# Optimization experiments

Measured on AMD Instinct MI355X. Metric: run time of the kernel, lower is better.

Reference implementation:

```python
import jax, jax.numpy as jnp
import numpy as np

NUM_HEADS = 8
D_HEAD = 64
LN_EPS = 1e-6


def _pad_idx(lengths, max_len):
    # flat indices into a [B*max_len, ...] dense buffer for each packed token
    return np.concatenate([b * max_len + np.arange(int(l)) for b, l in enumerate(lengths)])


def _layer_norm(x, scale, bias):
    mu = jnp.mean(x, axis=-1, keepdims=True)
    var = jnp.mean(jnp.square(x - mu), axis=-1, keepdims=True)
    return (x - mu) * jax.lax.rsqrt(var + LN_EPS) * scale + bias


def setup_inputs() -> dict:
    key = jax.random.key(0)
    ks = jax.random.split(key, 12)
    d_model, d_ff, H, dh = 512, 2048, NUM_HEADS, D_HEAD
    lengths = np.array([128 * (i + 1) for i in range(8)], dtype=np.int64)  # sum = 4608
    total = int(lengths.sum())
    s = 0.02
    return {
        "x": jax.random.normal(ks[0], (total, d_model), jnp.float32),
        "mem": jax.random.normal(ks[1], (total, d_model), jnp.float32),
        "lengths_x": lengths,
        "lengths_mem": lengths.copy(),
        "Wq": jax.random.normal(ks[2], (d_model, H * dh), jnp.float32) * s,
        "Wk": jax.random.normal(ks[3], (d_model, H * dh), jnp.float32) * s,
        "Wv": jax.random.normal(ks[4], (d_model, H * dh), jnp.float32) * s,
        "Wo": jax.random.normal(ks[5], (H * dh, d_model), jnp.float32) * s,
        "ln1_scale": jnp.ones((d_model,), jnp.float32),
        "ln1_bias": jnp.zeros((d_model,), jnp.float32),
        "W1": jax.random.normal(ks[6], (d_model, d_ff), jnp.float32) * s,
        "b1": jnp.zeros((d_ff,), jnp.float32),
        "W2": jax.random.normal(ks[7], (d_ff, d_model), jnp.float32) * s,
        "b2": jnp.zeros((d_model,), jnp.float32),
        "ln2_scale": jnp.ones((d_model,), jnp.float32),
        "ln2_bias": jnp.zeros((d_model,), jnp.float32),
    }


def reference(x, mem, lengths_x, lengths_mem, Wq, Wk, Wv, Wo,
              ln1_scale, ln1_bias, W1, b1, W2, b2, ln2_scale, ln2_bias):
    lx = np.asarray(lengths_x)
    lm = np.asarray(lengths_mem)
    B = lx.shape[0]
    Lx = int(lx.max())
    Lm = int(lm.max())
    H, dh = NUM_HEADS, D_HEAD

    idx_x = _pad_idx(lx, Lx)
    idx_m = _pad_idx(lm, Lm)

    def pad(packed, idx, B, L):
        dense = jnp.zeros((B * L,) + packed.shape[1:], packed.dtype).at[idx].set(packed)
        return dense.reshape((B, L) + packed.shape[1:])

    q = pad((x @ Wq).reshape(-1, H, dh), idx_x, B, Lx)   # [B, Lx, H, dh]
    k = pad((mem @ Wk).reshape(-1, H, dh), idx_m, B, Lm)  # [B, Lm, H, dh]
    v = pad((mem @ Wv).reshape(-1, H, dh), idx_m, B, Lm)

    e = jnp.einsum('bxhd,byhd->bhxy', q, k) / np.sqrt(dh)  # [B, H, Lx, Lm]
    # validity mask: (query pos < len_x) & (key pos < len_mem)
    mask = (np.arange(Lx)[None, :, None] < lx[:, None, None]) & \
           (np.arange(Lm)[None, None, :] < lm[:, None, None])
    mask = jnp.asarray(mask)[:, None, :, :]  # [B, 1, Lx, Lm]
    e = jnp.where(mask, e, jnp.float32(-1e30))  # finite -inf surrogate; identical softmax on valid rows
    alpha = jax.nn.softmax(e, axis=-1)
    out = jnp.einsum('bhxy,byhd->bxhd', alpha, v).reshape(B, Lx, H * dh)
    out = out @ Wo                                  # [B, Lx, d_model]
    out = out.reshape(B * Lx, -1)[idx_x]            # pack back to [total_x, d_model]

    h = _layer_norm(x + out, ln1_scale, ln1_bias)
    ffn = jax.nn.relu(h @ W1 + b1) @ W2 + b2
    return _layer_norm(h + ffn, ln2_scale, ln2_bias)
```

## Files before the change

kernel.cpp:

```cpp
#include <hip/hip_runtime.h>
#include <stdint.h>

typedef short bf8v __attribute__((ext_vector_type(8)));
typedef float f4v  __attribute__((ext_vector_type(4)));
typedef short s8v  __attribute__((ext_vector_type(8)));
typedef short s4v  __attribute__((ext_vector_type(4)));
typedef int   i2v  __attribute__((ext_vector_type(2)));

__device__ __forceinline__ float bf2f(short b){
  unsigned u = ((unsigned)(unsigned short)b) << 16;
  union { unsigned u; float f; } c; c.u = u; return c.f;
}
__device__ __forceinline__ short f2bf(float f){
  union { float f; unsigned u; } c; c.f = f;
  unsigned r = (c.u + 0x7FFFu + ((c.u >> 16) & 1u)) >> 16;
  return (short)r;
}
__device__ __forceinline__ void gload16(const short* g, short* l){
  __builtin_amdgcn_global_load_lds(
      (const __attribute__((address_space(1))) void*)g,
      (__attribute__((address_space(3))) void*)l, 16, 0, 0);
}

__global__ __launch_bounds__(256) void setup_kernel(
    const int* lx, const int* lm, int* meta,
    const float* __restrict__ Wq, const float* __restrict__ Wk,
    const float* __restrict__ Wv, const float* __restrict__ Wo,
    const float* __restrict__ W1, const float* __restrict__ W2,
    short* __restrict__ WqT, short* __restrict__ WkT,
    short* __restrict__ WvT, short* __restrict__ WoT,
    short* __restrict__ W1T, short* __restrict__ W2T){
  __shared__ int sjp[9], skvc[8];
  __shared__ float tile[32][33];
  int tid = threadIdx.x;
  int bid = blockIdx.x;

  if (bid == 0){
    if (tid == 0){
      int is64 = ((lx[1] | lx[3] | lx[5] | lx[7]) == 0) ? 1 : 0;
      int ox = 0, om = 0;
      for (int b = 0; b < 8; ++b){
        int a = is64 ? lx[2*b] : lx[b];
        int c = is64 ? lm[2*b] : lm[b];
        meta[b] = a; meta[8+b] = c;
        meta[16+b] = ox; meta[25+b] = om;
        ox += a; om += c;
      }
      meta[24] = ox; meta[33] = om;
      int jp = 0;
      for (int b = 0; b < 8; ++b){
        int Lm_ = meta[8+b];
        int kvc = (Lm_ + 255) / 256; if (kvc > 4) kvc = 4; if (kvc < 1) kvc = 1;
        int clen = (((Lm_ + kvc - 1) / kvc) + 31) & ~31;
        meta[34+b] = kvc; meta[42+b] = clen;
        meta[50+b] = jp;
        sjp[b] = jp; skvc[b] = kvc;
        int qt = (meta[b] + 63) / 64;
        jp += qt * kvc * 8;
      }
      meta[58] = jp;
      sjp[8] = jp;
    }
    __syncthreads();
    int njobs = sjp[8];
    for (int j = tid; j < njobs; j += blockDim.x){
      int b = 0;
      #pragma unroll
      for (int i = 1; i < 8; ++i) if (j >= sjp[i]) b = i;
      int local = j - sjp[b];
      int kvc = skvc[b];
      int h = local & 7;
      int r = local >> 3;
      int c = r % kvc;
      int qt = r / kvc;
      meta[64+j] = b | (h << 4) | (c << 7) | (qt << 11);
    }
    return;
  }

  int wbid = bid - 1;
  const float* W; short* WT; int K, N, t0;
  if      (wbid <  256){ W=Wq; WT=WqT; K=512;  N=512;  t0=0;    }
  else if (wbid <  512){ W=Wk; WT=WkT; K=512;  N=512;  t0=256;  }
  else if (wbid <  768){ W=Wv; WT=WvT; K=512;  N=512;  t0=512;  }
  else if (wbid < 1024){ W=Wo; WT=WoT; K=512;  N=512;  t0=768;  }
  else if (wbid < 2048){ W=W1; WT=W1T; K=512;  N=2048; t0=1024; }
  else                 { W=W2; WT=W2T; K=2048; N=512;  t0=2048; }
  int lt = wbid - t0;
  int ntn = N / 32;
  int tk = lt / ntn, tn = lt % ntn;
  int r0 = tid >> 5, c = tid & 31;
  #pragma unroll
  for (int i = 0; i < 4; ++i){
    int r = r0 + i*8;
    tile[r][c] = W[(long)(tk*32 + r)*N + tn*32 + c];
  }
  __syncthreads();
  #pragma unroll
  for (int i = 0; i < 4; ++i){
    int r = r0 + i*8;
    WT[(long)(tn*32 + r)*K + tk*32 + c] = f2bf(tile[c][r]);
  }
}

template<bool AF32>
__device__ __forceinline__ void stage_g64(const void* A, const short* Bt,
    long brow, long bcol, int M, int N, int K, int t,
    short* Als, short* Bls){
  int tid = threadIdx.x;
  {
    int row = tid >> 2, slot = tid & 3;
    int cg = slot ^ ((row >> 1) & 3);
    long ar = brow + row; if (ar >= M) ar = M - 1;
    if constexpr (AF32){
      const float* src = (const float*)A + ar*(long)K + t + cg*8;
      float4 f0 = *(const float4*)src;
      float4 f1 = *(const float4*)(src + 4);
      s8v o;
      o[0]=f2bf(f0.x); o[1]=f2bf(f0.y); o[2]=f2bf(f0.z); o[3]=f2bf(f0.w);
      o[4]=f2bf(f1.x); o[5]=f2bf(f1.y); o[6]=f2bf(f1.z); o[7]=f2bf(f1.w);
      *(s8v*)&Als[tid*8] = o;
    } else {
      gload16((const short*)A + ar*(long)K + t + cg*8, &Als[tid*8]);
    }
  }
  #pragma unroll
  for (int i = 0; i < 2; ++i){
    int cc = i*256 + tid;
    int row = cc >> 2, slot = cc & 3;
    int cg = slot ^ ((row >> 1) & 3);
    long br = bcol + row; if (br >= N) br = N - 1;
    gload16(Bt + br*(long)K + t + cg*8, &Bls[cc*8]);
  }
}

template<bool AF32>
__device__ __forceinline__ void gemm_core64(const void* A, const short* Bt,
    short* __restrict__ Cb, const float* __restrict__ bias,
    int M, int N, int K, int k0, int klen,
    float scale, int relu, int colmajor,
    long brow, long bcol, short* Als, short* Bls){
  int tid = threadIdx.x;
  int lane = tid & 63, w = tid >> 6;
  int wcol = w * 32;
  int l15 = lane & 15, l4 = lane >> 4;

  f4v acc[4][2];
  #pragma unroll
  for (int m = 0; m < 4; ++m)
    #pragma unroll
    for (int n = 0; n < 2; ++n) acc[m][n] = (f4v){0.f,0.f,0.f,0.f};

  int nt = klen / 32;
  stage_g64<AF32>(A, Bt, brow, bcol, M, N, K, k0, Als, Bls);
  for (int t = 0; t < nt; ++t){
    __syncthreads();
    if (t + 1 < nt)
      stage_g64<AF32>(A, Bt, brow, bcol, M, N, K, k0 + (t+1)*32,
                      Als + ((t+1)&1)*2048, Bls + ((t+1)&1)*4096);
    const short* Ab = Als + (t&1)*2048;
    const short* Bb = Bls + (t&1)*4096;
    bf8v a[4], b[2];
    #pragma unroll
    for (int m = 0; m < 4; ++m){
      int row = m*16 + l15;
      a[m] = *(const bf8v*)&Ab[row*32 + (l4 ^ ((row >> 1) & 3))*8];
    }
    #pragma unroll
    for (int n = 0; n < 2; ++n){
      int row = wcol + n*16 + l15;
      b[n] = *(const bf8v*)&Bb[row*32 + (l4 ^ ((row >> 1) & 3))*8];
    }
    #pragma unroll
    for (int m = 0; m < 4; ++m){
      acc[m][0] = __builtin_amdgcn_mfma_f32_16x16x32_bf16(a[m], b[0], acc[m][0], 0, 0, 0);
      acc[m][1] = __builtin_amdgcn_mfma_f32_16x16x32_bf16(a[m], b[1], acc[m][1], 0, 0, 0);
    }
  }

  #pragma unroll
  for (int m = 0; m < 4; ++m){
    #pragma unroll
    for (int n = 0; n < 2; ++n){
      long col = bcol + wcol + n*16 + l15;
      float bi = (bias != nullptr && col < N) ? bias[col] : 0.f;
      #pragma unroll
      for (int j = 0; j < 4; ++j){
        long row = brow + m*16 + 4*l4 + j;
        if (row < M && col < N){
          float v = acc[m][n][j] * scale + bi;
          if (relu) v = fmaxf(v, 0.f);
          Cb[colmajor ? (col*(long)M + row) : (row*(long)N + col)] = f2bf(v);
        }
      }
    }
  }
}

__global__ __launch_bounds__(256) void gemm64(
    const short* __restrict__ A, const short* __restrict__ Bt,
    short* __restrict__ C, const float* __restrict__ bias,
    int M, int N, int K, int klen, float scale, int relu, int colmajor){
  __shared__ __align__(16) short Als[2*64*32];
  __shared__ __align__(16) short Bls[2*128*32];
  int chunk = blockIdx.z;
  gemm_core64<false>(A, Bt, C + (long)chunk * M * N, bias, M, N, K, chunk*klen, klen,
                     scale, relu, colmajor,
                     (long)blockIdx.y * 64, (long)blockIdx.x * 128, Als, Bls);
}

__global__ __launch_bounds__(256) void gemm_qkv(
    const float* __restrict__ x, const float* __restrict__ mem,
    const short* __restrict__ WqT, const short* __restrict__ WkT,
    const short* __restrict__ WvT,
    short* __restrict__ Qb, short* __restrict__ Kbf, short* __restrict__ Vtb,
    int total){
  __shared__ __align__(16) short Als[2*64*32];
  __shared__ __align__(16) short Bls[2*128*32];
  int seg = blockIdx.x >> 2;
  const float* A  = (seg == 0) ? x : mem;
  const short* Bt = (seg == 0) ? WqT : ((seg == 1) ? WkT : WvT);
  short* C        = (seg == 0) ? Qb  : ((seg == 1) ? Kbf : Vtb);
  float scale     = (seg == 0) ? 0.125f : 1.f;
  int colmajor    = (seg == 2);
  gemm_core64<true>(A, Bt, C, nullptr, total, 512, 512, 0, 512, scale, 0, colmajor,
                    (long)blockIdx.y * 64, (long)(blockIdx.x & 3) * 128, Als, Bls);
}

__global__ __launch_bounds__(256) void attn_kernel(
    const short* __restrict__ Q, const short* __restrict__ Kb,
    const short* __restrict__ Vt, short* __restrict__ Ob,
    short* __restrict__ Opart, float* __restrict__ mlpart,
    const int* __restrict__ meta, int total){
  __shared__ __align__(16) short Kls[2][32*64];
  __shared__ __align__(16) short Vls[2][64*32];
  __shared__ __align__(16) short Pls[4][16*32];
  int tid = threadIdx.x;
  int lane = tid & 63, w = tid >> 6;
  int l15 = lane & 15, l4 = lane >> 4;
  int njobs = meta[58];

  for (int j = blockIdx.x; j < njobs; j += gridDim.x){
    int word = meta[64+j];
    int b = word & 15, h = (word >> 4) & 7, c = (word >> 7) & 15, qt = word >> 11;
    int Lx = meta[b], Lm = meta[8+b];
    int ox = meta[16+b], om = meta[25+b];
    int kvc = meta[34+b], clen = meta[42+b];
    int c0 = c * clen;
    int cend = c0 + clen; if (cend > Lm) cend = Lm;
    int nt = (cend - c0 + 31) / 32;
    int qbase = qt*64 + w*16;

    __syncthreads();

    #define ATTN_STAGE(T, BUF)                                                  \
      {                                                                         \
        int kv0_ = c0 + (T)*32;                                                 \
        int kr = tid >> 3, ks_ = tid & 7;                                       \
        int cgk = ks_ ^ (kr & 7);                                               \
        int ktok = kv0_ + kr; if (ktok >= Lm) ktok = Lm - 1;                    \
        gload16(Kb + (long)(om + ktok)*512 + h*64 + cgk*8, &Kls[BUF][tid*8]);   \
        int vr = tid >> 2, vs = tid & 3;                                        \
        int cgv = vs ^ (vr & 3);                                                \
        int vkv = kv0_ + cgv*8; if (vkv + 8 > Lm) vkv = Lm - 8;                 \
        gload16(Vt + (long)(h*64 + vr)*total + om + vkv, &Vls[BUF][tid*8]);     \
      }

    ATTN_STAGE(0, 0)

    int qr = qbase + l15;
    const short* qp = Q + (long)(ox + (qr < Lx ? qr : Lx - 1))*512 + h*64 + l4*8;
    bf8v aq0 = *(const bf8v*)qp;
    bf8v aq1 = *(const bf8v*)(qp + 32);

    float mrun = -1e30f, lrun = 0.f;
    f4v o[4];
    #pragma unroll
    for (int n = 0; n < 4; ++n) o[n] = (f4v){0.f,0.f,0.f,0.f};

    for (int t = 0; t < nt; ++t){
      __syncthreads();
      if (t + 1 < nt) ATTN_STAGE(t+1, (t+1)&1)
      int buf = t & 1;
      int kv0 = c0 + t*32;

      f4v s[2];
      #pragma unroll
      for (int n = 0; n < 2; ++n){
        int krow = n*16 + l15;
        bf8v k0 = *(const bf8v*)&Kls[buf][krow*64 + ((l4    ) ^ (krow & 7))*8];
        bf8v k1 = *(const bf8v*)&Kls[buf][krow*64 + ((4 + l4) ^ (krow & 7))*8];
        f4v z = (f4v){0.f,0.f,0.f,0.f};
        z = __builtin_amdgcn_mfma_f32_16x16x32_bf16(k0, aq0, z, 0, 0, 0);
        z = __builtin_amdgcn_mfma_f32_16x16x32_bf16(k1, aq1, z, 0, 0, 0);
        s[n] = z;
      }
      if (kv0 + 32 > cend){
        #pragma unroll
        for (int n = 0; n < 2; ++n){
          int kvb = kv0 + n*16 + 4*l4;
          #pragma unroll
          for (int jj = 0; jj < 4; ++jj)
            if (kvb + jj >= cend) s[n][jj] = -1e30f;
        }
      }
      float m1 = fmaxf(fmaxf(fmaxf(s[0][0], s[0][1]), fmaxf(s[0][2], s[0][3])),
                       fmaxf(fmaxf(s[1][0], s[1][1]), fmaxf(s[1][2], s[1][3])));
      m1 = fmaxf(m1, __shfl_xor(m1, 16, 64));
      m1 = fmaxf(m1, __shfl_xor(m1, 32, 64));
      float mnew = fmaxf(mrun, m1);
      float sc = __expf(mrun - mnew);
      mrun = mnew;
      float rs = 0.f;
      #pragma unroll
      for (int n = 0; n < 2; ++n)
        #pragma unroll
        for (int jj = 0; jj < 4; ++jj){
          float p = __expf(s[n][jj] - mnew);
          s[n][jj] = p; rs += p;
        }
      rs += __shfl_xor(rs, 16, 64);
      rs += __shfl_xor(rs, 32, 64);
      lrun = lrun * sc + rs;
      #pragma unroll
      for (int n = 0; n < 4; ++n) o[n] *= sc;

      #pragma unroll
      for (int n = 0; n < 2; ++n){
        unsigned r0, r1;
        asm("v_cvt_pk_bf16_f32 %0, %1, %2" : "=v"(r0) : "v"(s[n][0]), "v"(s[n][1]));
        asm("v_cvt_pk_bf16_f32 %0, %1, %2" : "=v"(r1) : "v"(s[n][2]), "v"(s[n][3]));
        i2v pr; pr[0] = (int)r0; pr[1] = (int)r1;
        int cs = (n*4 + l4) ^ ((l15 & 3) << 1);
        *(i2v*)&Pls[w][l15*32 + cs*4] = pr;
      }
      bf8v pb = *(const bf8v*)&Pls[w][l15*32 + (((2*l4) ^ ((l15 & 3) << 1))*4)];

      #pragma unroll
      for (int n2 = 0; n2 < 4; ++n2){
        int vrow = n2*16 + l15;
        bf8v vv = *(const bf8v*)&Vls[buf][vrow*32 + ((l4 ^ (vrow & 3))*8)];
        o[n2] = __builtin_amdgcn_mfma_f32_16x16x32_bf16(vv, pb, o[n2], 0, 0, 0);
      }
    }
    #undef ATTN_STAGE

    if (qr < Lx){
      if (kvc == 1){
        float inv = 1.f / lrun;
        long obase = (long)(ox + qr)*512 + h*64;
        #pragma unroll
        for (int n2 = 0; n2 < 4; ++n2){
          s4v ov;
          #pragma unroll
          for (int jj = 0; jj < 4; ++jj) ov[jj] = f2bf(o[n2][jj] * inv);
          *(s4v*)&Ob[obase + n2*16 + l4*4] = ov;
        }
      } else {
        long slot = ((long)(ox + qr)*8 + h)*4 + c;
        #pragma unroll
        for (int n2 = 0; n2 < 4; ++n2){
          s4v ov;
          #pragma unroll
          for (int jj = 0; jj < 4; ++jj) ov[jj] = f2bf(o[n2][jj]);
          *(s4v*)&Opart[slot*64 + n2*16 + l4*4] = ov;
        }
        if (l4 == 0){
          float2 ml; ml.x = mrun; ml.y = lrun;
          *(float2*)&mlpart[slot*2] = ml;
        }
      }
    }
  }
}

__global__ __launch_bounds__(256) void attn_combine(
    const short* __restrict__ Opart, const float* __restrict__ mlpart,
    short* __restrict__ Ob, const int* __restrict__ meta, int total){
  int w = threadIdx.x >> 6, lane = threadIdx.x & 63;
  int row = blockIdx.x*4 + w;
  if (row >= total) return;
  int b = 0;
  #pragma unroll
  for (int i = 1; i < 8; ++i) if (row >= meta[16+i]) b = i;
  int kvc = meta[34+b];
  if (kvc <= 1) return;
  for (int h = 0; h < 8; ++h){
    long sbase = ((long)row*8 + h)*4;
    float m_ = -1e30f;
    for (int c = 0; c < kvc; ++c) m_ = fmaxf(m_, mlpart[(sbase+c)*2]);
    float num = 0.f, den = 0.f;
    for (int c = 0; c < kvc; ++c){
      float mc = mlpart[(sbase+c)*2];
      float lc = mlpart[(sbase+c)*2 + 1];
      float wgt = __expf(mc - m_);
      num += wgt * bf2f(Opart[(sbase+c)*64 + lane]);
      den += wgt * lc;
    }
    Ob[(long)row*512 + h*64 + lane] = f2bf(num / den);
  }
}

__global__ __launch_bounds__(256) void ln_fuse(
    const float* __restrict__ Af, const short* __restrict__ Ab,
    const short* __restrict__ PartB, int nparts, long pstride,
    const float* __restrict__ bias,
    const float* __restrict__ gamma, const float* __restrict__ beta,
    short* __restrict__ outb, float* __restrict__ outf, int rows){
  int w = threadIdx.x >> 6, lane = threadIdx.x & 63;
  long row = (long)blockIdx.x * 4 + w;
  if (row >= rows) return;
  int c0 = lane * 8;
  long base = row * 512 + c0;
  float v[8];
  if (Af){
    float4 f0 = *(const float4*)(Af + base);
    float4 f1 = *(const float4*)(Af + base + 4);
    v[0]=f0.x; v[1]=f0.y; v[2]=f0.z; v[3]=f0.w;
    v[4]=f1.x; v[5]=f1.y; v[6]=f1.z; v[7]=f1.w;
  } else {
    s8v a = *(const s8v*)(Ab + base);
    #pragma unroll
    for (int j = 0; j < 8; ++j) v[j] = bf2f(a[j]);
  }
  for (int c = 0; c < nparts; ++c){
    s8v pv = *(const s8v*)(PartB + c*pstride + base);
    #pragma unroll
    for (int j = 0; j < 8; ++j) v[j] += bf2f(pv[j]);
  }
  if (bias){
    #pragma unroll
    for (int j = 0; j < 8; ++j) v[j] += bias[c0 + j];
  }
  float sum = 0.f;
  #pragma unroll
  for (int j = 0; j < 8; ++j) sum += v[j];
  #pragma unroll
  for (int m = 1; m < 64; m <<= 1) sum += __shfl_xor(sum, m, 64);
  float mu = sum * (1.f/512.f);
  float q = 0.f;
  #pragma unroll
  for (int j = 0; j < 8; ++j){ float d = v[j] - mu; q += d*d; }
  #pragma unroll
  for (int m = 1; m < 64; m <<= 1) q += __shfl_xor(q, m, 64);
  float rs = rsqrtf(q * (1.f/512.f) + 1e-6f);
  float ov[8];
  #pragma unroll
  for (int j = 0; j < 8; ++j)
    ov[j] = (v[j] - mu) * rs * gamma[c0 + j] + beta[c0 + j];
  if (outb){
    s8v os;
    #pragma unroll
    for (int j = 0; j < 8; ++j) os[j] = f2bf(ov[j]);
    *(s8v*)(outb + base) = os;
  }
  if (outf){
    float4 f0 = {ov[0], ov[1], ov[2], ov[3]};
    float4 f1 = {ov[4], ov[5], ov[6], ov[7]};
    *(float4*)(outf + base) = f0;
    *(float4*)(outf + base + 4) = f1;
  }
}

extern "C" void kernel_launch(void* const* d_in, const int* in_sizes, int n_in,
                              void* d_out, int out_size, void* d_ws, size_t ws_size,
                              hipStream_t stream){
  (void)n_in; (void)out_size; (void)ws_size;
  const float* x   = (const float*)d_in[0];
  const float* mem = (const float*)d_in[1];
  const int*   lxr = (const int*)d_in[2];
  const int*   lmr = (const int*)d_in[3];
  const float* Wq  = (const float*)d_in[4];
  const float* Wk  = (const float*)d_in[5];
  const float* Wv  = (const float*)d_in[6];
  const float* Wo  = (const float*)d_in[7];
  const float* g1  = (const float*)d_in[8];
  const float* be1 = (const float*)d_in[9];
  const float* W1  = (const float*)d_in[10];
  const float* b1  = (const float*)d_in[11];
  const float* W2  = (const float*)d_in[12];
  const float* b2  = (const float*)d_in[13];
  const float* g2  = (const float*)d_in[14];
  const float* be2 = (const float*)d_in[15];
  float* out = (float*)d_out;

  int total = in_sizes[0] / 512;
  if (total <= 0) return;
  long long n = (long long)total * 512;

  char* p = (char*)d_ws;
  int*   meta  = (int*)p;    p += 16384;
  short* Qb    = (short*)p;  p += n*2;
  short* Kbf   = (short*)p;  p += n*2;
  short* Vtb   = (short*)p;  p += n*2;
  short* attnb = (short*)p;  p += n*2;
  short* hb    = (short*)p;  p += n*2;
  short* ffn1  = (short*)p;  p += (long long)total*2048*2;
  short* Opart = (short*)p;  p += (long long)total*8*4*64*2;
  float* mlprt = (float*)p;  p += (long long)total*8*4*2*4;
  short* p_wo  = (short*)p;  p += n*4*2;
  short* p_ff  = (short*)p;  p += n*4*2;
  short* WqT   = (short*)p;  p += 512*512*2;
  short* WkT   = (short*)p;  p += 512*512*2;
  short* WvT   = (short*)p;  p += 512*512*2;
  short* WoT   = (short*)p;  p += 512*512*2;
  short* W1T   = (short*)p;  p += 2048*512*2;
  short* W2T   = (short*)p;  p += 512*2048*2;

  setup_kernel<<<dim3(1 + 3072), 256, 0, stream>>>(
      lxr, lmr, meta, Wq, Wk, Wv, Wo, W1, W2, WqT, WkT, WvT, WoT, W1T, W2T);

  int mt64 = (total + 63)/64;
  gemm_qkv<<<dim3(12, mt64), 256, 0, stream>>>(x, mem, WqT, WkT, WvT,
                                               Qb, Kbf, Vtb, total);

  attn_kernel<<<dim3(2048), 256, 0, stream>>>(Qb, Kbf, Vtb, attnb,
                                              Opart, mlprt, meta, total);
  attn_combine<<<dim3((unsigned)((total + 3)/4)), 256, 0, stream>>>(
      Opart, mlprt, attnb, meta, total);

  gemm64<<<dim3(4, mt64, 4), 256, 0, stream>>>(attnb, WoT, p_wo, nullptr,
                                               total, 512, 512, 128, 1.f, 0, 0);
  ln_fuse<<<dim3((unsigned)((total + 3)/4)), 256, 0, stream>>>(
      x, nullptr, p_wo, 4, n, nullptr, g1, be1, hb, nullptr, total);

  gemm64<<<dim3(16, mt64, 1), 256, 0, stream>>>(hb, W1T, ffn1, b1,
                                                total, 2048, 512, 512, 1.f, 1, 0);
  gemm64<<<dim3(4, mt64, 4), 256, 0, stream>>>(ffn1, W2T, p_ff, nullptr,
                                               total, 512, 2048, 512, 1.f, 0, 0);
  ln_fuse<<<dim3((unsigned)((total + 3)/4)), 256, 0, stream>>>(
      nullptr, hb, p_ff, 4, n, b2, g2, be2, nullptr, out, total);
}
```

Measured before the change: 178.1 us.

## Merge all stages into one cooperative persistent kernel with grid syncs

Replaces the chain of separate launches (weight transpose, QKV GEMM, attention, combine, Wo GEMM, LN, FFN GEMMs, LN) with a single cooperative persistent kernel. Blocks loop over the work items of each phase and use grid-wide syncs between phases. The goal is to remove per-launch overhead and the gaps between kernels. The Wo split-K factor also drops from 4 to 2. In exchange, the grid is capped at 1024 blocks, and grid syncs plus lower occupancy during heavy phases such as attention may cost throughput.

```diff
diff --git a/kernel.cpp b/kernel.cpp
--- a/kernel.cpp
+++ b/kernel.cpp
@@ -1,5 +1,8 @@
 #include <hip/hip_runtime.h>
+#include <hip/hip_cooperative_groups.h>
 #include <stdint.h>
+
+namespace cg = cooperative_groups;
 
 typedef short bf8v __attribute__((ext_vector_type(8)));
 typedef float f4v  __attribute__((ext_vector_type(4)));
@@ -22,26 +25,193 @@
       (__attribute__((address_space(3))) void*)l, 16, 0, 0);
 }
 
-__global__ __launch_bounds__(256) void setup_kernel(
-    const int* lx, const int* lm, int* meta,
-    const float* __restrict__ Wq, const float* __restrict__ Wk,
-    const float* __restrict__ Wv, const float* __restrict__ Wo,
-    const float* __restrict__ W1, const float* __restrict__ W2,
-    short* __restrict__ WqT, short* __restrict__ WkT,
-    short* __restrict__ WvT, short* __restrict__ WoT,
-    short* __restrict__ W1T, short* __restrict__ W2T){
-  __shared__ int sjp[9], skvc[8];
-  __shared__ float tile[32][33];
+struct MegaArgs {
+  const float* x; const float* mem;
+  const int* lx; const int* lm;
+  const float* Wq; const float* Wk; const float* Wv; const float* Wo;
+  const float* W1; const float* W2;
+  const float* g1; const float* be1; const float* b1;
+  const float* b2; const float* g2; const float* be2;
+  float* out;
+  int total;
+  int* meta;
+  short* Qb; short* Kbf; short* Vtb; short* attnb; short* hb; short* ffn1;
+  short* Opart; float* mlprt; short* p_wo; short* p_ff;
+  short* WqT; short* WkT; short* WvT; short* WoT; short* W1T; short* W2T;
+};
+
+template<bool AF32>
+__device__ __forceinline__ void stage_g64(const void* A, const short* Bt,
+    long brow, long bcol, int M, int N, int K, int t,
+    short* Als, short* Bls){
   int tid = threadIdx.x;
-  int bid = blockIdx.x;
+  {
+    int row = tid >> 2, slot = tid & 3;
+    int cg2 = slot ^ ((row >> 1) & 3);
+    long ar = brow + row; if (ar >= M) ar = M - 1;
+    if constexpr (AF32){
+      const float* src = (const float*)A + ar*(long)K + t + cg2*8;
+      float4 f0 = *(const float4*)src;
+      float4 f1 = *(const float4*)(src + 4);
+      s8v o;
+      o[0]=f2bf(f0.x); o[1]=f2bf(f0.y); o[2]=f2bf(f0.z); o[3]=f2bf(f0.w);
+      o[4]=f2bf(f1.x); o[5]=f2bf(f1.y); o[6]=f2bf(f1.z); o[7]=f2bf(f1.w);
+      *(s8v*)&Als[tid*8] = o;
+    } else {
+      gload16((const short*)A + ar*(long)K + t + cg2*8, &Als[tid*8]);
+    }
+  }
+  #pragma unroll
+  for (int i = 0; i < 2; ++i){
+    int cc = i*256 + tid;
+    int row = cc >> 2, slot = cc & 3;
+    int cg2 = slot ^ ((row >> 1) & 3);
+    long br = bcol + row; if (br >= N) br = N - 1;
+    gload16(Bt + br*(long)K + t + cg2*8, &Bls[cc*8]);
+  }
+}
+
+template<bool AF32>
+__device__ __forceinline__ void gemm_core64(const void* A, const short* Bt,
+    short* __restrict__ Cb, const float* __restrict__ bias,
+    int M, int N, int K, int k0, int klen,
+    float scale, int relu, int colmajor,
+    long brow, long bcol, short* Als, short* Bls){
+  int tid = threadIdx.x;
+  int lane = tid & 63, w = tid >> 6;
+  int wcol = w * 32;
+  int l15 = lane & 15, l4 = lane >> 4;
+
+  f4v acc[4][2];
+  #pragma unroll
+  for (int m = 0; m < 4; ++m)
+    #pragma unroll
+    for (int n = 0; n < 2; ++n) acc[m][n] = (f4v){0.f,0.f,0.f,0.f};
+
+  int nt = klen / 32;
+  stage_g64<AF32>(A, Bt, brow, bcol, M, N, K, k0, Als, Bls);
+  for (int t = 0; t < nt; ++t){
+    __syncthreads();
+    if (t + 1 < nt)
+      stage_g64<AF32>(A, Bt, brow, bcol, M, N, K, k0 + (t+1)*32,
+                      Als + ((t+1)&1)*2048, Bls + ((t+1)&1)*4096);
+    const short* Ab = Als + (t&1)*2048;
+    const short* Bb = Bls + (t&1)*4096;
+    bf8v a[4], b[2];
+    #pragma unroll
+    for (int m = 0; m < 4; ++m){
+      int row = m*16 + l15;
+      a[m] = *(const bf8v*)&Ab[row*32 + (l4 ^ ((row >> 1) & 3))*8];
+    }
+    #pragma unroll
+    for (int n = 0; n < 2; ++n){
+      int row = wcol + n*16 + l15;
+      b[n] = *(const bf8v*)&Bb[row*32 + (l4 ^ ((row >> 1) & 3))*8];
+    }
+    #pragma unroll
+    for (int m = 0; m < 4; ++m){
+      acc[m][0] = __builtin_amdgcn_mfma_f32_16x16x32_bf16(a[m], b[0], acc[m][0], 0, 0, 0);
+      acc[m][1] = __builtin_amdgcn_mfma_f32_16x16x32_bf16(a[m], b[1], acc[m][1], 0, 0, 0);
+    }
+  }
+
+  #pragma unroll
+  for (int m = 0; m < 4; ++m){
+    #pragma unroll
+    for (int n = 0; n < 2; ++n){
+      long col = bcol + wcol + n*16 + l15;
+      float bi = (bias != nullptr && col < N) ? bias[col] : 0.f;
+      #pragma unroll
+      for (int j = 0; j < 4; ++j){
+        long row = brow + m*16 + 4*l4 + j;
+        if (row < M && col < N){
+          float v = acc[m][n][j] * scale + bi;
+          if (relu) v = fmaxf(v, 0.f);
+          Cb[colmajor ? (col*(long)M + row) : (row*(long)N + col)] = f2bf(v);
+        }
+      }
+    }
+  }
+}
+
+__device__ __forceinline__ void ln_row(
+    const float* Af, const short* Ab, const short* PartB, int nparts,
+    long pstride, const float* bias, const float* gamma, const float* beta,
+    short* outb, float* outf, long row, int lane){
+  int c0 = lane * 8;
+  long base = row * 512 + c0;
+  float v[8];
+  if (Af){
+    float4 f0 = *(const float4*)(Af + base);
+    float4 f1 = *(const float4*)(Af + base + 4);
+    v[0]=f0.x; v[1]=f0.y; v[2]=f0.z; v[3]=f0.w;
+    v[4]=f1.x; v[5]=f1.y; v[6]=f1.z; v[7]=f1.w;
+  } else {
+    s8v a = *(const s8v*)(Ab + base);
+    #pragma unroll
+    for (int j = 0; j < 8; ++j) v[j] = bf2f(a[j]);
+  }
+  for (int c = 0; c < nparts; ++c){
+    s8v pv = *(const s8v*)(PartB + c*pstride + base);
+    #pragma unroll
+    for (int j = 0; j < 8; ++j) v[j] += bf2f(pv[j]);
+  }
+  if (bias){
+    #pragma unroll
+    for (int j = 0; j < 8; ++j) v[j] += bias[c0 + j];
+  }
+  float sum = 0.f;
+  #pragma unroll
+  for (int j = 0; j < 8; ++j) sum += v[j];
+  #pragma unroll
+  for (int m = 1; m < 64; m <<= 1) sum += __shfl_xor(sum, m, 64);
+  float mu = sum * (1.f/512.f);
+  float q = 0.f;
+  #pragma unroll
+  for (int j = 0; j < 8; ++j){ float d = v[j] - mu; q += d*d; }
+  #pragma unroll
+  for (int m = 1; m < 64; m <<= 1) q += __shfl_xor(q, m, 64);
+  float rs = rsqrtf(q * (1.f/512.f) + 1e-6f);
+  float ov[8];
+  #pragma unroll
+  for (int j = 0; j < 8; ++j)
+    ov[j] = (v[j] - mu) * rs * gamma[c0 + j] + beta[c0 + j];
+  if (outb){
+    s8v os;
+    #pragma unroll
+    for (int j = 0; j < 8; ++j) os[j] = f2bf(ov[j]);
+    *(s8v*)(outb + base) = os;
+  }
+  if (outf){
+    float4 f0 = {ov[0], ov[1], ov[2], ov[3]};
+    float4 f1 = {ov[4], ov[5], ov[6], ov[7]};
+    *(float4*)(outf + base) = f0;
+    *(float4*)(outf + base + 4) = f1;
+  }
+}
+
+__global__ __launch_bounds__(256, 4) void mega_kernel(MegaArgs A){
+  __shared__ __align__(16) char sm[24576];
+  short* Als = (short*)sm;
+  short* Bls = (short*)(sm + 8192);
+  cg::grid_group gg = cg::this_grid();
+
+  int tid = threadIdx.x, bid = blockIdx.x, G = (int)gridDim.x;
+  int lane = tid & 63, w = tid >> 6;
+  int l15 = lane & 15, l4 = lane >> 4;
+  int total = A.total;
+  long long n = (long long)total * 512;
+  int mt64 = (total + 63) / 64;
+  int* meta = A.meta;
 
   if (bid == 0){
+    __shared__ int sjp[9], skvc[8];
     if (tid == 0){
-      int is64 = ((lx[1] | lx[3] | lx[5] | lx[7]) == 0) ? 1 : 0;
+      int is64 = ((A.lx[1] | A.lx[3] | A.lx[5] | A.lx[7]) == 0) ? 1 : 0;
       int ox = 0, om = 0;
       for (int b = 0; b < 8; ++b){
-        int a = is64 ? lx[2*b] : lx[b];
-        int c = is64 ? lm[2*b] : lm[b];
+        int a = is64 ? A.lx[2*b] : A.lx[b];
+        int c = is64 ? A.lm[2*b] : A.lm[b];
         meta[b] = a; meta[8+b] = c;
         meta[16+b] = ox; meta[25+b] = om;
         ox += a; om += c;
@@ -75,390 +245,282 @@
       int qt = r / kvc;
       meta[64+j] = b | (h << 4) | (c << 7) | (qt << 11);
     }
-    return;
-  }
-
-  int wbid = bid - 1;
-  const float* W; short* WT; int K, N, t0;
-  if      (wbid <  256){ W=Wq; WT=WqT; K=512;  N=512;  t0=0;    }
-  else if (wbid <  512){ W=Wk; WT=WkT; K=512;  N=512;  t0=256;  }
-  else if (wbid <  768){ W=Wv; WT=WvT; K=512;  N=512;  t0=512;  }
-  else if (wbid < 1024){ W=Wo; WT=WoT; K=512;  N=512;  t0=768;  }
-  else if (wbid < 2048){ W=W1; WT=W1T; K=512;  N=2048; t0=1024; }
-  else                 { W=W2; WT=W2T; K=2048; N=512;  t0=2048; }
-  int lt = wbid - t0;
-  int ntn = N / 32;
-  int tk = lt / ntn, tn = lt % ntn;
-  int r0 = tid >> 5, c = tid & 31;
-  #pragma unroll
-  for (int i = 0; i < 4; ++i){
-    int r = r0 + i*8;
-    tile[r][c] = W[(long)(tk*32 + r)*N + tn*32 + c];
-  }
-  __syncthreads();
-  #pragma unroll
-  for (int i = 0; i < 4; ++i){
-    int r = r0 + i*8;
-    WT[(long)(tn*32 + r)*K + tk*32 + c] = f2bf(tile[c][r]);
-  }
-}
-
-template<bool AF32>
-__device__ __forceinline__ void stage_g64(const void* A, const short* Bt,
-    long brow, long bcol, int M, int N, int K, int t,
-    short* Als, short* Bls){
-  int tid = threadIdx.x;
-  {
-    int row = tid >> 2, slot = tid & 3;
-    int cg = slot ^ ((row >> 1) & 3);
-    long ar = brow + row; if (ar >= M) ar = M - 1;
-    if constexpr (AF32){
-      const float* src = (const float*)A + ar*(long)K + t + cg*8;
-      float4 f0 = *(const float4*)src;
-      float4 f1 = *(const float4*)(src + 4);
-      s8v o;
-      o[0]=f2bf(f0.x); o[1]=f2bf(f0.y); o[2]=f2bf(f0.z); o[3]=f2bf(f0.w);
-      o[4]=f2bf(f1.x); o[5]=f2bf(f1.y); o[6]=f2bf(f1.z); o[7]=f2bf(f1.w);
-      *(s8v*)&Als[tid*8] = o;
-    } else {
-      gload16((const short*)A + ar*(long)K + t + cg*8, &Als[tid*8]);
-    }
-  }
-  #pragma unroll
-  for (int i = 0; i < 2; ++i){
-    int cc = i*256 + tid;
-    int row = cc >> 2, slot = cc & 3;
-    int cg = slot ^ ((row >> 1) & 3);
-    long br = bcol + row; if (br >= N) br = N - 1;
-    gload16(Bt + br*(long)K + t + cg*8, &Bls[cc*8]);
-  }
-}
-
-template<bool AF32>
-__device__ __forceinline__ void gemm_core64(const void* A, const short* Bt,
-    short* __restrict__ Cb, const float* __restrict__ bias,
-    int M, int N, int K, int k0, int klen,
-    float scale, int relu, int colmajor,
-    long brow, long bcol, short* Als, short* Bls){
-  int tid = threadIdx.x;
-  int lane = tid & 63, w = tid >> 6;
-  int wcol = w * 32;
-  int l15 = lane & 15, l4 = lane >> 4;
-
-  f4v acc[4][2];
-  #pragma unroll
-  for (int m = 0; m < 4; ++m)
-    #pragma unroll
-    for (int n = 0; n < 2; ++n) acc[m][n] = (f4v){0.f,0.f,0.f,0.f};
-
-  int nt = klen / 32;
-  stage_g64<AF32>(A, Bt, brow, bcol, M, N, K, k0, Als, Bls);
-  for (int t = 0; t < nt; ++t){
-    __syncthreads();
-    if (t + 1 < nt)
-      stage_g64<AF32>(A, Bt, brow, bcol, M, N, K, k0 + (t+1)*32,
-                      Als + ((t+1)&1)*2048, Bls + ((t+1)&1)*4096);
-    const short* Ab = Als + (t&1)*2048;
-    const short* Bb = Bls + (t&1)*4096;
-    bf8v a[4], b[2];
-    #pragma unroll
-    for (int m = 0; m < 4; ++m){
-      int row = m*16 + l15;
-      a[m] = *(const bf8v*)&Ab[row*32 + (l4 ^ ((row >> 1) & 3))*8];
-    }
-    #pragma unroll
-    for (int n = 0; n < 2; ++n){
-      int row = wcol + n*16 + l15;
-      b[n] = *(const bf8v*)&Bb[row*32 + (l4 ^ ((row >> 1) & 3))*8];
-    }
-    #pragma unroll
-    for (int m = 0; m < 4; ++m){
-      acc[m][0] = __builtin_amdgcn_mfma_f32_16x16x32_bf16(a[m], b[0], acc[m][0], 0, 0, 0);
-      acc[m][1] = __builtin_amdgcn_mfma_f32_16x16x32_bf16(a[m], b[1], acc[m][1], 0, 0, 0);
-    }
-  }
-
-  #pragma unroll
-  for (int m = 0; m < 4; ++m){
-    #pragma unroll
-    for (int n = 0; n < 2; ++n){
-      long col = bcol + wcol + n*16 + l15;
-      float bi = (bias != nullptr && col < N) ? bias[col] : 0.f;
+  } else {
+    float (*tile)[33] = (float(*)[33])sm;
+    for (int wb = bid - 1; wb < 3072; wb += G - 1){
+      const float* W; short* WT; int K, N, t0;
+      if      (wb <  256){ W=A.Wq; WT=A.WqT; K=512;  N=512;  t0=0;    }
+      else if (wb <  512){ W=A.Wk; WT=A.WkT; K=512;  N=512;  t0=256;  }
+      else if (wb <  768){ W=A.Wv; WT=A.WvT; K=512;  N=512;  t0=512;  }
+      else if (wb < 1024){ W=A.Wo; WT=A.WoT; K=512;  N=512;  t0=768;  }
+      else if (wb < 2048){ W=A.W1; WT=A.W1T; K=512;  N=2048; t0=1024; }
+      else               { W=A.W2; WT=A.W2T; K=2048; N=512;  t0=2048; }
+      int lt = wb - t0;
+      int ntn = N / 32;
+      int tk = lt / ntn, tn = lt % ntn;
+      int r0 = tid >> 5, c = tid & 31;
       #pragma unroll
-      for (int j = 0; j < 4; ++j){
-        long row = brow + m*16 + 4*l4 + j;
-        if (row < M && col < N){
-          float v = acc[m][n][j] * scale + bi;
-          if (relu) v = fmaxf(v, 0.f);
-          Cb[colmajor ? (col*(long)M + row) : (row*(long)N + col)] = f2bf(v);
-        }
-      }
-    }
-  }
-}
-
-__global__ __launch_bounds__(256) void gemm64(
-    const short* __restrict__ A, const short* __restrict__ Bt,
-    short* __restrict__ C, const float* __restrict__ bias,
-    int M, int N, int K, int klen, float scale, int relu, int colmajor){
-  __shared__ __align__(16) short Als[2*64*32];
-  __shared__ __align__(16) short Bls[2*128*32];
-  int chunk = blockIdx.z;
-  gemm_core64<false>(A, Bt, C + (long)chunk * M * N, bias, M, N, K, chunk*klen, klen,
-                     scale, relu, colmajor,
-                     (long)blockIdx.y * 64, (long)blockIdx.x * 128, Als, Bls);
-}
-
-__global__ __launch_bounds__(256) void gemm_qkv(
-    const float* __restrict__ x, const float* __restrict__ mem,
-    const short* __restrict__ WqT, const short* __restrict__ WkT,
-    const short* __restrict__ WvT,
-    short* __restrict__ Qb, short* __restrict__ Kbf, short* __restrict__ Vtb,
-    int total){
-  __shared__ __align__(16) short Als[2*64*32];
-  __shared__ __align__(16) short Bls[2*128*32];
-  int seg = blockIdx.x >> 2;
-  const float* A  = (seg == 0) ? x : mem;
-  const short* Bt = (seg == 0) ? WqT : ((seg == 1) ? WkT : WvT);
-  short* C        = (seg == 0) ? Qb  : ((seg == 1) ? Kbf : Vtb);
-  float scale     = (seg == 0) ? 0.125f : 1.f;
-  int colmajor    = (seg == 2);
-  gemm_core64<true>(A, Bt, C, nullptr, total, 512, 512, 0, 512, scale, 0, colmajor,
-                    (long)blockIdx.y * 64, (long)(blockIdx.x & 3) * 128, Als, Bls);
-}
-
-__global__ __launch_bounds__(256) void attn_kernel(
-    const short* __restrict__ Q, const short* __restrict__ Kb,
-    const short* __restrict__ Vt, short* __restrict__ Ob,
-    short* __restrict__ Opart, float* __restrict__ mlpart,
-    const int* __restrict__ meta, int total){
-  __shared__ __align__(16) short Kls[2][32*64];
-  __shared__ __align__(16) short Vls[2][64*32];
-  __shared__ __align__(16) short Pls[4][16*32];
-  int tid = threadIdx.x;
-  int lane = tid & 63, w = tid >> 6;
-  int l15 = lane & 15, l4 = lane >> 4;
-  int njobs = meta[58];
-
-  for (int j = blockIdx.x; j < njobs; j += gridDim.x){
-    int word = meta[64+j];
-    int b = word & 15, h = (word >> 4) & 7, c = (word >> 7) & 15, qt = word >> 11;
-    int Lx = meta[b], Lm = meta[8+b];
-    int ox = meta[16+b], om = meta[25+b];
-    int kvc = meta[34+b], clen = meta[42+b];
-    int c0 = c * clen;
-    int cend = c0 + clen; if (cend > Lm) cend = Lm;
-    int nt = (cend - c0 + 31) / 32;
-    int qbase = qt*64 + w*16;
-
-    __syncthreads();
-
-    #define ATTN_STAGE(T, BUF)                                                  \
-      {                                                                         \
-        int kv0_ = c0 + (T)*32;                                                 \
-        int kr = tid >> 3, ks_ = tid & 7;                                       \
-        int cgk = ks_ ^ (kr & 7);                                               \
-        int ktok = kv0_ + kr; if (ktok >= Lm) ktok = Lm - 1;                    \
-        gload16(Kb + (long)(om + ktok)*512 + h*64 + cgk*8, &Kls[BUF][tid*8]);   \
-        int vr = tid >> 2, vs = tid & 3;                                        \
-        int cgv = vs ^ (vr & 3);                                                \
-        int vkv = kv0_ + cgv*8; if (vkv + 8 > Lm) vkv = Lm - 8;                 \
-        gload16(Vt + (long)(h*64 + vr)*total + om + vkv, &Vls[BUF][tid*8]);     \
-      }
-
-    ATTN_STAGE(0, 0)
-
-    int qr = qbase + l15;
-    const short* qp = Q + (long)(ox + (qr < Lx ? qr : Lx - 1))*512 + h*64 + l4*8;
-    bf8v aq0 = *(const bf8v*)qp;
-    bf8v aq1 = *(const bf8v*)(qp + 32);
-
-    float mrun = -1e30f, lrun = 0.f;
-    f4v o[4];
-    #pragma unroll
-    for (int n = 0; n < 4; ++n) o[n] = (f4v){0.f,0.f,0.f,0.f};
-
-    for (int t = 0; t < nt; ++t){
-      __syncthreads();
-      if (t + 1 < nt) ATTN_STAGE(t+1, (t+1)&1)
-      int buf = t & 1;
-      int kv0 = c0 + t*32;
-
-      f4v s[2];
+      for (int i = 0; i < 4; ++i){
+        int r = r0 + i*8;
+        tile[r][c] = W[(long)(tk*32 + r)*N + tn*32 + c];
+      }
+      __syncthreads();
       #pragma unroll
-      for (int n = 0; n < 2; ++n){
-        int krow = n*16 + l15;
-        bf8v k0 = *(const bf8v*)&Kls[buf][krow*64 + ((l4    ) ^ (krow & 7))*8];
-        bf8v k1 = *(const bf8v*)&Kls[buf][krow*64 + ((4 + l4) ^ (krow & 7))*8];
-        f4v z = (f4v){0.f,0.f,0.f,0.f};
-        z = __builtin_amdgcn_mfma_f32_16x16x32_bf16(k0, aq0, z, 0, 0, 0);
-        z = __builtin_amdgcn_mfma_f32_16x16x32_bf16(k1, aq1, z, 0, 0, 0);
-        s[n] = z;
-      }
-      if (kv0 + 32 > cend){
+      for (int i = 0; i < 4; ++i){
+        int r = r0 + i*8;
+        WT[(long)(tn*32 + r)*K + tk*32 + c] = f2bf(tile[c][r]);
+      }
+      __syncthreads();
+    }
+  }
+  gg.sync();
+
+  {
+    int njobs = 12 * mt64;
+    for (int j = bid; j < njobs; j += G){
+      int xx = j % 12, row = j / 12;
+      int seg = xx >> 2;
+      const void* Af  = (seg == 0) ? (const void*)A.x : (const void*)A.mem;
+      const short* Bt = (seg == 0) ? A.WqT : ((seg == 1) ? A.WkT : A.WvT);
+      short* C        = (seg == 0) ? A.Qb  : ((seg == 1) ? A.Kbf : A.Vtb);
+      float scale     = (seg == 0) ? 0.125f : 1.f;
+      int colmajor    = (seg == 2);
+      __syncthreads();
+      gemm_core64<true>(Af, Bt, C, nullptr, total, 512, 512, 0, 512,
+                        scale, 0, colmajor, (long)row*64, (long)(xx & 3)*128,
+                        Als, Bls);
+    }
+  }
+  gg.sync();
+
+  {
+    short (*Kls)[32*64] = (short(*)[32*64])sm;
+    short (*Vls)[64*32] = (short(*)[64*32])(sm + 8192);
+    short (*Pls)[16*32] = (short(*)[16*32])(sm + 16384);
+    int njobs = meta[58];
+    for (int j = bid; j < njobs; j += G){
+      int word = meta[64+j];
+      int b = word & 15, h = (word >> 4) & 7, c = (word >> 7) & 15, qt = word >> 11;
+      int Lx = meta[b], Lm = meta[8+b];
+      int ox = meta[16+b], om = meta[25+b];
+      int kvc = meta[34+b], clen = meta[42+b];
+      int c0 = c * clen;
+      int cend = c0 + clen; if (cend > Lm) cend = Lm;
+      int nt = (cend - c0 + 31) / 32;
+      int qbase = qt*64 + w*16;
+
+      __syncthreads();
+
+      #define ATTN_STAGE(T, BUF)                                                \
+        {                                                                       \
+          int kv0_ = c0 + (T)*32;                                               \
+          int kr = tid >> 3, ks_ = tid & 7;                                     \
+          int cgk = ks_ ^ (kr & 7);                                             \
+          int ktok = kv0_ + kr; if (ktok >= Lm) ktok = Lm - 1;                  \
+          gload16(A.Kbf + (long)(om + ktok)*512 + h*64 + cgk*8, &Kls[BUF][tid*8]); \
+          int vr = tid >> 2, vs = tid & 3;                                      \
+          int cgv = vs ^ (vr & 3);                                              \
+          int vkv = kv0_ + cgv*8; if (vkv + 8 > Lm) vkv = Lm - 8;               \
+          gload16(A.Vtb + (long)(h*64 + vr)*total + om + vkv, &Vls[BUF][tid*8]); \
+        }
+
+      ATTN_STAGE(0, 0)
+
+      int qr = qbase + l15;
+      const short* qp = A.Qb + (long)(ox + (qr < Lx ? qr : Lx - 1))*512 + h*64 + l4*8;
+      bf8v aq0 = *(const bf8v*)qp;
+      bf8v aq1 = *(const bf8v*)(qp + 32);
+
+      float mrun = -1e30f, lrun = 0.f;
+      f4v o[4];
+      #pragma unroll
+      for (int nn = 0; nn < 4; ++nn) o[nn] = (f4v){0.f,0.f,0.f,0.f};
+
+      for (int t = 0; t < nt; ++t){
+        __syncthreads();
+        if (t + 1 < nt) ATTN_STAGE(t+1, (t+1)&1)
+        int buf = t & 1;
+        int kv0 = c0 + t*32;
+
+        f4v s[2];
         #pragma unroll
-        for (int n = 0; n < 2; ++n){
-          int kvb = kv0 + n*16 + 4*l4;
+        for (int nn = 0; nn < 2; ++nn){
+          int krow = nn*16 + l15;
+          bf8v k0 = *(const bf8v*)&Kls[buf][krow*64 + ((l4    ) ^ (krow & 7))*8];
+          bf8v k1 = *(const bf8v*)&Kls[buf][krow*64 + ((4 + l4) ^ (krow & 7))*8];
+          f4v z = (f4v){0.f,0.f,0.f,0.f};
+          z = __builtin_amdgcn_mfma_f32_16x16x32_bf16(k0, aq0, z, 0, 0, 0);
+          z = __builtin_amdgcn_mfma_f32_16x16x32_bf16(k1, aq1, z, 0, 0, 0);
+          s[nn] = z;
+        }
+        if (kv0 + 32 > cend){
           #pragma unroll
-          for (int jj = 0; jj < 4; ++jj)
-            if (kvb + jj >= cend) s[n][jj] = -1e30f;
-        }
-      }
-      float m1 = fmaxf(fmaxf(fmaxf(s[0][0], s[0][1]), fmaxf(s[0][2], s[0][3])),
-                       fmaxf(fmaxf(s[1][0], s[1][1]), fmaxf(s[1][2], s[1][3])));
-      m1 = fmaxf(m1, __shfl_xor(m1, 16, 64));
-      m1 = fmaxf(m1, __shfl_xor(m1, 32, 64));
-      float mnew = fmaxf(mrun, m1);
-      float sc = __expf(mrun - mnew);
-      mrun = mnew;
-      float rs = 0.f;
-      #pragma unroll
-      for (int n = 0; n < 2; ++n)
+          for (int nn = 0; nn < 2; ++nn){
+            int kvb = kv0 + nn*16 + 4*l4;
+            #pragma unroll
+            for (int jj = 0; jj < 4; ++jj)
+              if (kvb + jj >= cend) s[nn][jj] = -1e30f;
+          }
+        }
+        float m1 = fmaxf(fmaxf(fmaxf(s[0][0], s[0][1]), fmaxf(s[0][2], s[0][3])),
+                         fmaxf(fmaxf(s[1][0], s[1][1]), fmaxf(s[1][2], s[1][3])));
+        m1 = fmaxf(m1, __shfl_xor(m1, 16, 64));
+        m1 = fmaxf(m1, __shfl_xor(m1, 32, 64));
+        float mnew = fmaxf(mrun, m1);
+        float sc = __expf(mrun - mnew);
+        mrun = mnew;
+        float rs = 0.f;
         #pragma unroll
-        for (int jj = 0; jj < 4; ++jj){
-          float p = __expf(s[n][jj] - mnew);
-          s[n][jj] = p; rs += p;
-        }
-      rs += __shfl_xor(rs, 16, 64);
-      rs += __shfl_xor(rs, 32, 64);
-      lrun = lrun * sc + rs;
-      #pragma unroll
-      for (int n = 0; n < 4; ++n) o[n] *= sc;
-
-      #pragma unroll
-      for (int n = 0; n < 2; ++n){
-        unsigned r0, r1;
-        asm("v_cvt_pk_bf16_f32 %0, %1, %2" : "=v"(r0) : "v"(s[n][0]), "v"(s[n][1]));
-        asm("v_cvt_pk_bf16_f32 %0, %1, %2" : "=v"(r1) : "v"(s[n][2]), "v"(s[n][3]));
-        i2v pr; pr[0] = (int)r0; pr[1] = (int)r1;
-        int cs = (n*4 + l4) ^ ((l15 & 3) << 1);
-        *(i2v*)&Pls[w][l15*32 + cs*4] = pr;
-      }
-      bf8v pb = *(const bf8v*)&Pls[w][l15*32 + (((2*l4) ^ ((l15 & 3) << 1))*4)];
-
-      #pragma unroll
-      for (int n2 = 0; n2 < 4; ++n2){
-        int vrow = n2*16 + l15;
-        bf8v vv = *(const bf8v*)&Vls[buf][vrow*32 + ((l4 ^ (vrow & 3))*8)];
-        o[n2] = __builtin_amdgcn_mfma_f32_16x16x32_bf16(vv, pb, o[n2], 0, 0, 0);
-      }
-    }
-    #undef ATTN_STAGE
-
-    if (qr < Lx){
-      if (kvc == 1){
-        float inv = 1.f / lrun;
-        long obase = (long)(ox + qr)*512 + h*64;
+        for (int nn = 0; nn < 2; ++nn)
+          #pragma unroll
+          for (int jj = 0; jj < 4; ++jj){
+            float pe = __expf(s[nn][jj] - mnew);
+            s[nn][jj] = pe; rs += pe;
+          }
+        rs += __shfl_xor(rs, 16, 64);
+        rs += __shfl_xor(rs, 32, 64);
+        lrun = lrun * sc + rs;
+        #pragma unroll
+        for (int nn = 0; nn < 4; ++nn) o[nn] *= sc;
+
+        #pragma unroll
+        for (int nn = 0; nn < 2; ++nn){
+          unsigned r0, r1;
+          asm("v_cvt_pk_bf16_f32 %0, %1, %2" : "=v"(r0) : "v"(s[nn][0]), "v"(s[nn][1]));
+          asm("v_cvt_pk_bf16_f32 %0, %1, %2" : "=v"(r1) : "v"(s[nn][2]), "v"(s[nn][3]));
+          i2v pr; pr[0] = (int)r0; pr[1] = (int)r1;
+          int cs = (nn*4 + l4) ^ ((l15 & 3) << 1);
+          *(i2v*)&Pls[w][l15*32 + cs*4] = pr;
+        }
+        bf8v pb = *(const bf8v*)&Pls[w][l15*32 + (((2*l4) ^ ((l15 & 3) << 1))*4)];
+
         #pragma unroll
         for (int n2 = 0; n2 < 4; ++n2){
-          s4v ov;
+          int vrow = n2*16 + l15;
+          bf8v vv = *(const bf8v*)&Vls[buf][vrow*32 + ((l4 ^ (vrow & 3))*8)];
+          o[n2] = __builtin_amdgcn_mfma_f32_16x16x32_bf16(vv, pb, o[n2], 0, 0, 0);
+        }
+      }
+      #undef ATTN_STAGE
+
+      if (qr < Lx){
+        if (kvc == 1){
+          float inv = 1.f / lrun;
+          long obase = (long)(ox + qr)*512 + h*64;
           #pragma unroll
-          for (int jj = 0; jj < 4; ++jj) ov[jj] = f2bf(o[n2][jj] * inv);
-          *(s4v*)&Ob[obase + n2*16 + l4*4] = ov;
-        }
-      } else {
-        long slot = ((long)(ox + qr)*8 + h)*4 + c;
+          for (int n2 = 0; n2 < 4; ++n2){
+            s4v ov;
+            #pragma unroll
+            for (int jj = 0; jj < 4; ++jj) ov[jj] = f2bf(o[n2][jj] * inv);
+            *(s4v*)&A.attnb[obase + n2*16 + l4*4] = ov;
+          }
+        } else {
+          long slot = ((long)(ox + qr)*8 + h)*4 + c;
+          #pragma unroll
+          for (int n2 = 0; n2 < 4; ++n2){
+            s4v ov;
+            #pragma unroll
+            for (int jj = 0; jj < 4; ++jj) ov[jj] = f2bf(o[n2][jj]);
+            *(s4v*)&A.Opart[slot*64 + n2*16 + l4*4] = ov;
+          }
+          if (l4 == 0){
+            float2 ml; ml.x = mrun; ml.y = lrun;
+            *(float2*)&A.mlprt[slot*2] = ml;
+          }
+        }
+      }
+    }
+  }
+  gg.sync();
+
+  {
+    int nr4 = (total + 3) >> 2;
+    for (int r4 = bid; r4 < nr4; r4 += G){
+      int row = r4*4 + w;
+      if (row < total){
+        int b = 0;
         #pragma unroll
-        for (int n2 = 0; n2 < 4; ++n2){
-          s4v ov;
-          #pragma unroll
-          for (int jj = 0; jj < 4; ++jj) ov[jj] = f2bf(o[n2][jj]);
-          *(s4v*)&Opart[slot*64 + n2*16 + l4*4] = ov;
-        }
-        if (l4 == 0){
-          float2 ml; ml.x = mrun; ml.y = lrun;
-          *(float2*)&mlpart[slot*2] = ml;
-        }
-      }
-    }
-  }
-}
-
-__global__ __launch_bounds__(256) void attn_combine(
-    const short* __restrict__ Opart, const float* __restrict__ mlpart,
-    short* __restrict__ Ob, const int* __restrict__ meta, int total){
-  int w = threadIdx.x >> 6, lane = threadIdx.x & 63;
-  int row = blockIdx.x*4 + w;
-  if (row >= total) return;
-  int b = 0;
-  #pragma unroll
-  for (int i = 1; i < 8; ++i) if (row >= meta[16+i]) b = i;
-  int kvc = meta[34+b];
-  if (kvc <= 1) return;
-  for (int h = 0; h < 8; ++h){
-    long sbase = ((long)row*8 + h)*4;
-    float m_ = -1e30f;
-    for (int c = 0; c < kvc; ++c) m_ = fmaxf(m_, mlpart[(sbase+c)*2]);
-    float num = 0.f, den = 0.f;
-    for (int c = 0; c < kvc; ++c){
-      float mc = mlpart[(sbase+c)*2];
-      float lc = mlpart[(sbase+c)*2 + 1];
-      float wgt = __expf(mc - m_);
-      num += wgt * bf2f(Opart[(sbase+c)*64 + lane]);
-      den += wgt * lc;
-    }
-    Ob[(long)row*512 + h*64 + lane] = f2bf(num / den);
-  }
-}
-
-__global__ __launch_bounds__(256) void ln_fuse(
-    const float* __restrict__ Af, const short* __restrict__ Ab,
-    const short* __restrict__ PartB, int nparts, long pstride,
-    const float* __restrict__ bias,
-    const float* __restrict__ gamma, const float* __restrict__ beta,
-    short* __restrict__ outb, float* __restrict__ outf, int rows){
-  int w = threadIdx.x >> 6, lane = threadIdx.x & 63;
-  long row = (long)blockIdx.x * 4 + w;
-  if (row >= rows) return;
-  int c0 = lane * 8;
-  long base = row * 512 + c0;
-  float v[8];
-  if (Af){
-    float4 f0 = *(const float4*)(Af + base);
-    float4 f1 = *(const float4*)(Af + base + 4);
-    v[0]=f0.x; v[1]=f0.y; v[2]=f0.z; v[3]=f0.w;
-    v[4]=f1.x; v[5]=f1.y; v[6]=f1.z; v[7]=f1.w;
-  } else {
-    s8v a = *(const s8v*)(Ab + base);
-    #pragma unroll
-    for (int j = 0; j < 8; ++j) v[j] = bf2f(a[j]);
-  }
-  for (int c = 0; c < nparts; ++c){
-    s8v pv = *(const s8v*)(PartB + c*pstride + base);
-    #pragma unroll
-    for (int j = 0; j < 8; ++j) v[j] += bf2f(pv[j]);
-  }
-  if (bias){
-    #pragma unroll
-    for (int j = 0; j < 8; ++j) v[j] += bias[c0 + j];
-  }
-  float sum = 0.f;
-  #pragma unroll
-  for (int j = 0; j < 8; ++j) sum += v[j];
-  #pragma unroll
-  for (int m = 1; m < 64; m <<= 1) sum += __shfl_xor(sum, m, 64);
-  float mu = sum * (1.f/512.f);
-  float q = 0.f;
-  #pragma unroll
-  for (int j = 0; j < 8; ++j){ float d = v[j] - mu; q += d*d; }
-  #pragma unroll
-  for (int m = 1; m < 64; m <<= 1) q += __shfl_xor(q, m, 64);
-  float rs = rsqrtf(q * (1.f/512.f) + 1e-6f);
-  float ov[8];
-  #pragma unroll
-  for (int j = 0; j < 8; ++j)
-    ov[j] = (v[j] - mu) * rs * gamma[c0 + j] + beta[c0 + j];
-  if (outb){
-    s8v os;
-    #pragma unroll
-    for (int j = 0; j < 8; ++j) os[j] = f2bf(ov[j]);
-    *(s8v*)(outb + base) = os;
-  }
-  if (outf){
-    float4 f0 = {ov[0], ov[1], ov[2], ov[3]};
-    float4 f1 = {ov[4], ov[5], ov[6], ov[7]};
-    *(float4*)(outf + base) = f0;
-    *(float4*)(outf + base + 4) = f1;
+        for (int i = 1; i < 8; ++i) if (row >= meta[16+i]) b = i;
+        int kvc = meta[34+b];
+        if (kvc > 1){
+          for (int h = 0; h < 8; ++h){
+            long sbase = ((long)row*8 + h)*4;
+            float m_ = -1e30f;
+            for (int c = 0; c < kvc; ++c) m_ = fmaxf(m_, A.mlprt[(sbase+c)*2]);
+            float num = 0.f, den = 0.f;
+            for (int c = 0; c < kvc; ++c){
+              float mc = A.mlprt[(sbase+c)*2];
+              float lc = A.mlprt[(sbase+c)*2 + 1];
+              float wgt = __expf(mc - m_);
+              num += wgt * bf2f(A.Opart[(sbase+c)*64 + lane]);
+              den += wgt * lc;
+            }
+            A.attnb[(long)row*512 + h*64 + lane] = f2bf(num / den);
+          }
+        }
+      }
+    }
+  }
+  gg.sync();
+
+  {
+    int njobs = 4 * mt64 * 2;
+    for (int j = bid; j < njobs; j += G){
+      int xx = j % 4;
+      int r = j / 4;
+      int row = r % mt64, chunk = r / mt64;
+      __syncthreads();
+      gemm_core64<false>(A.attnb, A.WoT, A.p_wo + (long)chunk * n, nullptr,
+                         total, 512, 512, chunk*256, 256, 1.f, 0, 0,
+                         (long)row*64, (long)xx*128, Als, Bls);
+    }
+  }
+  gg.sync();
+
+  {
+    int nr4 = (total + 3) >> 2;
+    for (int r4 = bid; r4 < nr4; r4 += G){
+      long row = (long)r4*4 + w;
+      if (row < total)
+        ln_row(A.x, nullptr, A.p_wo, 2, n, nullptr, A.g1, A.be1,
+               A.hb, nullptr, row, lane);
+    }
+  }
+  gg.sync();
+
+  {
+    int njobs = 16 * mt64;
+    for (int j = bid; j < njobs; j += G){
+      int xx = j % 16, row = j / 16;
+      __syncthreads();
+      gemm_core64<false>(A.hb, A.W1T, A.ffn1, A.b1, total, 2048, 512, 0, 512,
+                         1.f, 1, 0, (long)row*64, (long)xx*128, Als, Bls);
+    }
+  }
+  gg.sync();
+
+  {
+    int njobs = 4 * mt64 * 4;
+    for (int j = bid; j < njobs; j += G){
+      int xx = j % 4;
+      int r = j / 4;
+      int row = r % mt64, chunk = r / mt64;
+      __syncthreads();
+      gemm_core64<false>(A.ffn1, A.W2T, A.p_ff + (long)chunk * n, nullptr,
+                         total, 512, 2048, chunk*512, 512, 1.f, 0, 0,
+                         (long)row*64, (long)xx*128, Als, Bls);
+    }
+  }
+  gg.sync();
+
+  {
+    int nr4 = (total + 3) >> 2;
+    for (int r4 = bid; r4 < nr4; r4 += G){
+      long row = (long)r4*4 + w;
+      if (row < total)
+        ln_row(nullptr, A.hb, A.p_ff, 4, n, A.b2, A.g2, A.be2,
+               nullptr, A.out, row, lane);
+    }
   }
 }
 
@@ -466,24 +528,6 @@
                               void* d_out, int out_size, void* d_ws, size_t ws_size,
                               hipStream_t stream){
   (void)n_in; (void)out_size; (void)ws_size;
-  const float* x   = (const float*)d_in[0];
-  const float* mem = (const float*)d_in[1];
-  const int*   lxr = (const int*)d_in[2];
-  const int*   lmr = (const int*)d_in[3];
-  const float* Wq  = (const float*)d_in[4];
-  const float* Wk  = (const float*)d_in[5];
-  const float* Wv  = (const float*)d_in[6];
-  const float* Wo  = (const float*)d_in[7];
-  const float* g1  = (const float*)d_in[8];
-  const float* be1 = (const float*)d_in[9];
-  const float* W1  = (const float*)d_in[10];
-  const float* b1  = (const float*)d_in[11];
-  const float* W2  = (const float*)d_in[12];
-  const float* b2  = (const float*)d_in[13];
-  const float* g2  = (const float*)d_in[14];
-  const float* be2 = (const float*)d_in[15];
-  float* out = (float*)d_out;
-
   int total = in_sizes[0] / 512;
   if (total <= 0) return;
   long long n = (long long)total * 512;
@@ -498,7 +542,7 @@
   short* ffn1  = (short*)p;  p += (long long)total*2048*2;
   short* Opart = (short*)p;  p += (long long)total*8*4*64*2;
   float* mlprt = (float*)p;  p += (long long)total*8*4*2*4;
-  short* p_wo  = (short*)p;  p += n*4*2;
+  short* p_wo  = (short*)p;  p += n*2*2;
   short* p_ff  = (short*)p;  p += n*4*2;
   short* WqT   = (short*)p;  p += 512*512*2;
   short* WkT   = (short*)p;  p += 512*512*2;
@@ -507,27 +551,39 @@
   short* W1T   = (short*)p;  p += 2048*512*2;
   short* W2T   = (short*)p;  p += 512*2048*2;
 
-  setup_kernel<<<dim3(1 + 3072), 256, 0, stream>>>(
-      lxr, lmr, meta, Wq, Wk, Wv, Wo, W1, W2, WqT, WkT, WvT, WoT, W1T, W2T);
-
-  int mt64 = (total + 63)/64;
-  gemm_qkv<<<dim3(12, mt64), 256, 0, stream>>>(x, mem, WqT, WkT, WvT,
-                                               Qb, Kbf, Vtb, total);
-
-  attn_kernel<<<dim3(2048), 256, 0, stream>>>(Qb, Kbf, Vtb, attnb,
-                                              Opart, mlprt, meta, total);
-  attn_combine<<<dim3((unsigned)((total + 3)/4)), 256, 0, stream>>>(
-      Opart, mlprt, attnb, meta, total);
-
-  gemm64<<<dim3(4, mt64, 4), 256, 0, stream>>>(attnb, WoT, p_wo, nullptr,
-                                               total, 512, 512, 128, 1.f, 0, 0);
-  ln_fuse<<<dim3((unsigned)((total + 3)/4)), 256, 0, stream>>>(
-      x, nullptr, p_wo, 4, n, nullptr, g1, be1, hb, nullptr, total);
-
-  gemm64<<<dim3(16, mt64, 1), 256, 0, stream>>>(hb, W1T, ffn1, b1,
-                                                total, 2048, 512, 512, 1.f, 1, 0);
-  gemm64<<<dim3(4, mt64, 4), 256, 0, stream>>>(ffn1, W2T, p_ff, nullptr,
-                                               total, 512, 2048, 512, 1.f, 0, 0);
-  ln_fuse<<<dim3((unsigned)((total + 3)/4)), 256, 0, stream>>>(
-      nullptr, hb, p_ff, 4, n, b2, g2, be2, nullptr, out, total);
-}
+  MegaArgs ha;
+  ha.x   = (const float*)d_in[0];
+  ha.mem = (const float*)d_in[1];
+  ha.lx  = (const int*)d_in[2];
+  ha.lm  = (const int*)d_in[3];
+  ha.Wq  = (const float*)d_in[4];
+  ha.Wk  = (const float*)d_in[5];
+  ha.Wv  = (const float*)d_in[6];
+  ha.Wo  = (const float*)d_in[7];
+  ha.g1  = (const float*)d_in[8];
+  ha.be1 = (const float*)d_in[9];
+  ha.W1  = (const float*)d_in[10];
+  ha.b1  = (const float*)d_in[11];
+  ha.W2  = (const float*)d_in[12];
+  ha.b2  = (const float*)d_in[13];
+  ha.g2  = (const float*)d_in[14];
+  ha.be2 = (const float*)d_in[15];
+  ha.out = (float*)d_out;
+  ha.total = total;
+  ha.meta = meta;
+  ha.Qb = Qb; ha.Kbf = Kbf; ha.Vtb = Vtb; ha.attnb = attnb; ha.hb = hb;
+  ha.ffn1 = ffn1; ha.Opart = Opart; ha.mlprt = mlprt;
+  ha.p_wo = p_wo; ha.p_ff = p_ff;
+  ha.WqT = WqT; ha.WkT = WkT; ha.WvT = WvT; ha.WoT = WoT;
+  ha.W1T = W1T; ha.W2T = W2T;
+
+  int maxb = 0;
+  hipOccupancyMaxActiveBlocksPerMultiprocessor(&maxb, (const void*)mega_kernel, 256, 0);
+  if (maxb < 1) maxb = 1;
+  int G = maxb * 256;
+  if (G > 1024) G = 1024;
+
+  void* params[] = { (void*)&ha };
+  hipLaunchCooperativeKernel((const void*)mega_kernel, dim3((unsigned)G),
+                             dim3(256), params, 0, stream);
+}
```

Result: slower. 694.4 us (+289.9%).
